# Optimization experiments

Measured on AMD Instinct MI355X. Metric: run time of the kernel, lower is better.

The kernel has to match this reference:

```python
import jax, jax.numpy as jnp
import numpy as np
from jax import lax

EPS = 1e-5  # torch LayerNorm / BatchNorm1d default eps
HEADS, DH, DEPTH, C = 4, 128, 2, 512


def setup_inputs() -> dict:
    key = jax.random.key(0)
    ks = iter(jax.random.split(key, 48))
    def rn(shape, scale=1.0):
        return jax.random.normal(next(ks), shape, jnp.float32) * scale
    d, L = 1024, DEPTH
    inp = {}
    inp['x'] = rn((16, 10, 256, d))                      # (b, ncrops, T, d)
    # Temporal embedding: Conv1d(d -> 512, k=3, pad=1) + ReLU
    inp['W_emb'] = rn((C, d, 3), (d * 3) ** -0.5)
    inp['b_emb'] = jnp.zeros((C,), jnp.float32)
    # Transformer (depth=2), params stacked along layer axis
    inp['ln1_g'] = jnp.ones((L, C), jnp.float32); inp['ln1_b'] = jnp.zeros((L, C), jnp.float32)
    inp['W_qkv'] = rn((L, C, 4 * HEADS * DH), C ** -0.5)  # to_qkv (no bias), inner_dim*4 = 2048
    inp['W_o']  = rn((L, 2 * HEADS * DH, C), (2 * HEADS * DH) ** -0.5)
    inp['b_o']  = jnp.zeros((L, C), jnp.float32)
    inp['ln2_g'] = jnp.ones((L, C), jnp.float32); inp['ln2_b'] = jnp.zeros((L, C), jnp.float32)
    inp['W_f1'] = rn((L, C, C), C ** -0.5); inp['b_f1'] = jnp.zeros((L, C), jnp.float32)
    inp['W_f2'] = rn((L, C, C), C ** -0.5); inp['b_f2'] = jnp.zeros((L, C), jnp.float32)
    # NormalHead: conv1 512->32 (k=1), bn1, conv2 32->16 (k=1), bn2, conv3 16->1 (k=1)
    inp['c1_W'] = rn((32, C), C ** -0.5); inp['c1_b'] = jnp.zeros((32,), jnp.float32)
    inp['bn1_g'] = jnp.ones((32,), jnp.float32); inp['bn1_b'] = jnp.zeros((32,), jnp.float32)
    inp['bn1_m'] = rn((32,), 0.1)
    inp['bn1_v'] = jax.random.uniform(next(ks), (32,), jnp.float32, 0.5, 1.5)
    inp['c2_W'] = rn((16, 32), 32 ** -0.5); inp['c2_b'] = jnp.zeros((16,), jnp.float32)
    inp['bn2_g'] = jnp.ones((16,), jnp.float32); inp['bn2_b'] = jnp.zeros((16,), jnp.float32)
    inp['bn2_m'] = rn((16,), 0.1)
    inp['bn2_v'] = jax.random.uniform(next(ks), (16,), jnp.float32, 0.5, 1.5)
    inp['c3_W'] = rn((1, 16), 0.25); inp['c3_b'] = jnp.zeros((1,), jnp.float32)
    return inp


def _ln(z, g, b):
    m = z.mean(-1, keepdims=True)
    v = ((z - m) ** 2).mean(-1, keepdims=True)
    return (z - m) / jnp.sqrt(v + EPS) * g + b


def _bn_eval(z, g, b, m, v):  # z: (B, C, T), eval-mode BatchNorm1d
    return (z - m[None, :, None]) / jnp.sqrt(v[None, :, None] + EPS) * g[None, :, None] + b[None, :, None]


def _k1conv(z, W, b):  # pointwise Conv1d: z (B, Ci, T), W (Co, Ci)
    return jnp.einsum('bct,oc->bot', z, W) + b[None, :, None]


def reference(x, W_emb, b_emb, ln1_g, ln1_b, W_qkv, W_o, b_o, ln2_g, ln2_b,
              W_f1, b_f1, W_f2, b_f2, c1_W, c1_b, bn1_g, bn1_b, bn1_m, bn1_v,
              c2_W, c2_b, bn2_g, bn2_b, bn2_m, bn2_v, c3_W, c3_b):
    b, n, T, d = x.shape
    h = x.reshape(b * n, T, d)
    # Temporal embedding: Conv1d(k=3, pad=1) + ReLU
    h = lax.conv_general_dilated(h.transpose(0, 2, 1), W_emb, (1,), 'SAME',
                                 dimension_numbers=('NCH', 'OIH', 'NCH'))
    h = jax.nn.relu(h + b_emb[None, :, None]).transpose(0, 2, 1)  # (BN, T, 512)

    # fixed positional-decay attention map attn2 (T, T), batch-independent
    idx = jnp.arange(T, dtype=jnp.float32)
    tg = jnp.abs(idx[None, :] - idx[:, None])
    a2 = jnp.exp(-tg / jnp.exp(1.0))
    a2 = a2 / a2.sum(-1)  # NOTE: broadcast over last axis, exactly as in the torch code

    scale = DH ** -0.5
    for l in range(DEPTH):
        z = _ln(h, ln1_g[l], ln1_b[l])
        qkvt = z @ W_qkv[l]                                   # (BN, T, 2048)
        q, k, v, t = jnp.split(qkvt, 4, axis=-1)
        def to_heads(u):
            return u.reshape(u.shape[0], T, HEADS, DH).transpose(0, 2, 1, 3)
        q, k, v, t = map(to_heads, (q, k, v, t))              # (BN, H, T, DH)
        attn1 = jax.nn.softmax(jnp.einsum('bhid,bhjd->bhij', q, k) * scale, axis=-1)
        o1 = jnp.einsum('bhij,bhjd->bhid', attn1, v)
        o2 = jnp.einsum('ij,bhjd->bhid', a2, t)
        o = jnp.concatenate([o1, o2], axis=-1)                # (BN, H, T, 2*DH)
        o = o.transpose(0, 2, 1, 3).reshape(h.shape[0], T, HEADS * 2 * DH)
        h = o @ W_o[l] + b_o[l] + h                           # attn residual
        z = _ln(h, ln2_g[l], ln2_b[l])
        h = (jax.nn.gelu(z @ W_f1[l] + b_f1[l], approximate=False) @ W_f2[l] + b_f2[l]) + h

    # NormalHead on (BN, C, T)
    f = h.transpose(0, 2, 1)
    x1 = _k1conv(f, c1_W, c1_b)                               # (BN, 32, T)
    x2 = _k1conv(jax.nn.relu(_bn_eval(x1, bn1_g, bn1_b, bn1_m, bn1_v)), c2_W, c2_b)  # (BN, 16, T)
    scores = jax.nn.sigmoid(_k1conv(jax.nn.relu(_bn_eval(x2, bn2_g, bn2_b, bn2_m, bn2_v)), c3_W, c3_b))
    normal_scores = scores.reshape(b, n, T).mean(1)           # mean over ncrops -> (b, T)

    def maha(feats, anchor, var):  # Mahalanobis distance vs BN running stats (no eps, as in source)
        dist = jnp.sqrt(jnp.sum((feats - anchor[None, :, None]) ** 2 / var[None, :, None], axis=1))
        return dist.reshape(b, n, T).mean(1)

    distance_sum = maha(x1, bn1_m, bn1_v) + maha(x2, bn2_m, bn2_v)
    return distance_sum * normal_scores                       # (b, T)
```

## Files before the change

### kernel.cpp

```cpp
#include <hip/hip_runtime.h>
#include <math.h>

#define T_    256
#define D_    1024
#define C_    512
#define H_    4
#define DH_   128
#define BNB   160
#define LEPS  1e-5f
#define INV_E 0.36787944117144233f
#define SCALE_ 0.08838834764831845f
#define LDT   40

typedef unsigned short ushort;
typedef unsigned int   uint;
typedef __attribute__((ext_vector_type(8))) short short8;
typedef __attribute__((ext_vector_type(4))) float f32x4;

__device__ __forceinline__ ushort f2b(float f) {
    uint u = __float_as_uint(f);
    u += 0x7fffu + ((u >> 16) & 1u);
    return (ushort)(u >> 16);
}
__device__ __forceinline__ float b2f(ushort u) {
    return __uint_as_float(((uint)u) << 16);
}
__device__ __forceinline__ uint pk(float a, float b) {
    return (uint)f2b(a) | ((uint)f2b(b) << 16);
}

__global__ void zero_k(float* __restrict__ p, int n) {
    int i = blockIdx.x * 256 + threadIdx.x;
    if (i < n) p[i] = 0.0f;
}

__global__ void xcvt_k(const float* __restrict__ src, ushort* __restrict__ dst, int n4) {
    int i = blockIdx.x * 256 + threadIdx.x;
    if (i < n4) {
        float4 f = ((const float4*)src)[i];
        uint2 v;
        v.x = pk(f.x, f.y);
        v.y = pk(f.z, f.w);
        ((uint2*)dst)[i] = v;
    }
}

__global__ void tconv_k(const float* __restrict__ src, ushort* __restrict__ dst,
                        int K, int N) {
    int idx = blockIdx.x * 256 + threadIdx.x;
    if (idx >= N * K) return;
    int n = idx / K, k = idx % K;
    dst[idx] = f2b(src[(size_t)k * N + n]);
}

__global__ void bcvt_k(const float* __restrict__ src, ushort* __restrict__ dst, int n) {
    int i = blockIdx.x * 256 + threadIdx.x;
    if (i < n) dst[i] = f2b(src[i]);
}

__global__ void wemb_k(const float* __restrict__ W, ushort* __restrict__ Wt) {
    int idx = blockIdx.x * 256 + threadIdx.x;
    if (idx >= C_ * 3072) return;
    int c = idx / 3072, k = idx % 3072;
    int dt = k >> 10, ci = k & 1023;
    Wt[idx] = f2b(W[(size_t)c * 3072 + ci * 3 + dt]);
}

__global__ void a2_colsum_k(float* __restrict__ s) {
    int j = threadIdx.x;
    float acc = 0.0f;
    for (int k = 0; k < T_; k++) acc += expf(-fabsf((float)(j - k)) * INV_E);
    s[j] = acc;
}

__global__ void a2fill_k(const float* __restrict__ s, ushort* __restrict__ A2) {
    int i = blockIdx.x, j = threadIdx.x;
    A2[i * 256 + j] = f2b(expf(-fabsf((float)(i - j)) * INV_E) / s[j]);
}

__global__ __launch_bounds__(256)
void ln_k(const ushort* __restrict__ X, const float* __restrict__ g,
          const float* __restrict__ b, ushort* __restrict__ Z) {
    int row = blockIdx.x;
    int tid = threadIdx.x;
    const ushort* xr = X + (size_t)row * C_;
    float x0 = b2f(xr[tid]), x1 = b2f(xr[tid + 256]);
    __shared__ float red[256];
    red[tid] = x0 + x1;
    __syncthreads();
    for (int s = 128; s >= 1; s >>= 1) {
        if (tid < s) red[tid] += red[tid + s];
        __syncthreads();
    }
    float mean = red[0] * (1.0f / C_);
    __syncthreads();
    float d0 = x0 - mean, d1 = x1 - mean;
    red[tid] = d0 * d0 + d1 * d1;
    __syncthreads();
    for (int s = 128; s >= 1; s >>= 1) {
        if (tid < s) red[tid] += red[tid + s];
        __syncthreads();
    }
    float rinv = rsqrtf(red[0] * (1.0f / C_) + LEPS);
    ushort* zr = Z + (size_t)row * C_;
    zr[tid]       = f2b(d0 * rinv * g[tid]       + b[tid]);
    zr[tid + 256] = f2b(d1 * rinv * g[tid + 256] + b[tid + 256]);
}

template<int CONV, int ACT, int RESID, int OUTBF>
__global__ __launch_bounds__(256)
void gemm_k(const ushort* __restrict__ A, const ushort* __restrict__ B,
            const float* __restrict__ bias, const ushort* __restrict__ R,
            void* __restrict__ Cout, int M, int N, int K,
            const ushort* __restrict__ Xb) {
    __shared__ __align__(16) ushort As[128 * LDT];
    __shared__ __align__(16) ushort Bs[128 * LDT];
    const int tid  = threadIdx.x;
    const int lane = tid & 63, wave = tid >> 6;
    const int wr = wave >> 1, wc = wave & 1;
    const int lm = lane & 15, quad = lane >> 4;

    const int NP = gridDim.x, My = gridDim.y;
    int m_idx, n_idx;
    if ((My & 7) == 0) {
        int bid = blockIdx.y * NP + blockIdx.x;
        m_idx = (bid & 7) + 8 * (bid / (8 * NP));
        n_idx = (bid >> 3) % NP;
    } else {
        m_idx = blockIdx.y; n_idx = blockIdx.x;
    }
    const int m0 = m_idx * 128, n0 = n_idx * 128;
    const int r  = tid >> 1;
    const int c0 = (tid & 1) * 2;

    f32x4 acc[4][4];
#pragma unroll
    for (int mt = 0; mt < 4; mt++)
#pragma unroll
        for (int nt = 0; nt < 4; nt++) acc[mt][nt] = (f32x4){0.f, 0.f, 0.f, 0.f};

    for (int k0 = 0; k0 < K; k0 += 32) {
        if (CONV) {
            int g = m0 + r, bn = g >> 8, t = g & 255;
#pragma unroll
            for (int cc = 0; cc < 2; cc++) {
                int c = c0 + cc;
                int kc = k0 + c * 8;
                int dt = kc >> 10, ci = kc & 1023;
                int tt = t + dt - 1;
                uint4 val;
                if (tt >= 0 && tt < T_) {
                    val = *(const uint4*)(Xb + ((size_t)bn * T_ + tt) * D_ + ci);
                } else {
                    val.x = 0u; val.y = 0u; val.z = 0u; val.w = 0u;
                }
                *(uint4*)&As[r * LDT + c * 8] = val;
            }
        } else {
            const ushort* Arow = A + (size_t)(m0 + r) * K + k0;
            *(uint4*)&As[r * LDT + c0 * 8]       = *(const uint4*)(Arow + c0 * 8);
            *(uint4*)&As[r * LDT + (c0 + 1) * 8] = *(const uint4*)(Arow + (c0 + 1) * 8);
        }
        {
            const ushort* Brow = B + (size_t)(n0 + r) * K + k0;
            *(uint4*)&Bs[r * LDT + c0 * 8]       = *(const uint4*)(Brow + c0 * 8);
            *(uint4*)&Bs[r * LDT + (c0 + 1) * 8] = *(const uint4*)(Brow + (c0 + 1) * 8);
        }
        __syncthreads();
        short8 af[4], bfv[4];
#pragma unroll
        for (int mt = 0; mt < 4; mt++)
            af[mt] = *(const short8*)&As[(wr * 64 + mt * 16 + lm) * LDT + quad * 8];
#pragma unroll
        for (int nt = 0; nt < 4; nt++)
            bfv[nt] = *(const short8*)&Bs[(wc * 64 + nt * 16 + lm) * LDT + quad * 8];
#pragma unroll
        for (int mt = 0; mt < 4; mt++)
#pragma unroll
            for (int nt = 0; nt < 4; nt++)
                acc[mt][nt] = __builtin_amdgcn_mfma_f32_16x16x32_bf16(
                    af[mt], bfv[nt], acc[mt][nt], 0, 0, 0);
        __syncthreads();
    }

#pragma unroll
    for (int mt = 0; mt < 4; mt++) {
        int grow0 = m0 + wr * 64 + mt * 16 + quad * 4;
#pragma unroll
        for (int nt = 0; nt < 4; nt++) {
            int gcol = n0 + wc * 64 + nt * 16 + lm;
            float bia = bias ? bias[gcol] : 0.0f;
            f32x4 v = acc[mt][nt];
#pragma unroll
            for (int i = 0; i < 4; i++) {
                int grow = grow0 + i;
                float val = v[i] + bia;
                if (ACT == 1) val = val * 0.5f * (1.0f + erff(val * 0.70710678118654752f));
                if (ACT == 2) val = fmaxf(val, 0.0f);
                if (RESID) val += b2f(R[(size_t)grow * N + gcol]);
                if (OUTBF) ((ushort*)Cout)[(size_t)grow * N + gcol] = f2b(val);
                else       ((float*)Cout)[(size_t)grow * N + gcol]  = val;
            }
        }
    }
}

__global__ __launch_bounds__(256)
void attn1_k(const ushort* __restrict__ qkvt, ushort* __restrict__ O) {
    const int bn = blockIdx.x, h = blockIdx.y;
    const int tid = threadIdx.x;
    const int wave = tid >> 6, lane = tid & 63;
    const int lm = lane & 15, quad = lane >> 4;
    __shared__ __align__(16) ushort Ks[32 * 136];
    __shared__ __align__(16) ushort Vt[128 * 40];
    __shared__ __align__(16) ushort Ps[4][64 * 40];
    const ushort* base = qkvt + (size_t)bn * T_ * 2048;

    short8 aq[4][4];
#pragma unroll
    for (int mt = 0; mt < 4; mt++) {
        const ushort* qrow = base + (size_t)(wave * 64 + mt * 16 + lm) * 2048 + h * DH_;
#pragma unroll
        for (int ks = 0; ks < 4; ks++)
            aq[mt][ks] = *(const short8*)(qrow + ks * 32 + quad * 8);
    }

    f32x4 oacc[4][8];
#pragma unroll
    for (int mt = 0; mt < 4; mt++)
#pragma unroll
        for (int nt = 0; nt < 8; nt++) oacc[mt][nt] = (f32x4){0.f, 0.f, 0.f, 0.f};
    float mrow[4][4], lrow[4][4];
#pragma unroll
    for (int mt = 0; mt < 4; mt++)
#pragma unroll
        for (int i = 0; i < 4; i++) { mrow[mt][i] = -1e30f; lrow[mt][i] = 0.0f; }

    for (int kt = 0; kt < 8; kt++) {
        __syncthreads();
#pragma unroll
        for (int u = 0; u < 2; u++) {
            int ii = tid + u * 256;
            int j = ii >> 4, dc = ii & 15;
            *(uint4*)&Ks[j * 136 + dc * 8] =
                *(const uint4*)(base + (size_t)(kt * 32 + j) * 2048 + 512 + h * DH_ + dc * 8);
        }
        {
            int j = tid & 31, half = tid >> 5;
            const ushort* vrow = base + (size_t)(kt * 32 + j) * 2048 + 1024 + h * DH_ + half * 16;
            uint4 v0 = *(const uint4*)vrow;
            uint4 v1 = *(const uint4*)(vrow + 8);
            ushort e[16];
            *(uint4*)&e[0] = v0; *(uint4*)&e[8] = v1;
#pragma unroll
            for (int u = 0; u < 16; u++)
                Vt[(half * 16 + u) * 40 + j] = e[u];
        }
        __syncthreads();

        f32x4 s[4][2];
#pragma unroll
        for (int mt = 0; mt < 4; mt++)
#pragma unroll
            for (int nt = 0; nt < 2; nt++) s[mt][nt] = (f32x4){0.f, 0.f, 0.f, 0.f};
#pragma unroll
        for (int ks = 0; ks < 4; ks++) {
            short8 bk0 = *(const short8*)&Ks[lm * 136 + ks * 32 + quad * 8];
            short8 bk1 = *(const short8*)&Ks[(16 + lm) * 136 + ks * 32 + quad * 8];
#pragma unroll
            for (int mt = 0; mt < 4; mt++) {
                s[mt][0] = __builtin_amdgcn_mfma_f32_16x16x32_bf16(aq[mt][ks], bk0, s[mt][0], 0, 0, 0);
                s[mt][1] = __builtin_amdgcn_mfma_f32_16x16x32_bf16(aq[mt][ks], bk1, s[mt][1], 0, 0, 0);
            }
        }

#pragma unroll
        for (int mt = 0; mt < 4; mt++) {
#pragma unroll
            for (int i = 0; i < 4; i++) {
                float v0 = s[mt][0][i] * SCALE_;
                float v1 = s[mt][1][i] * SCALE_;
                float rmax = fmaxf(v0, v1);
#pragma unroll
                for (int mk = 1; mk < 16; mk <<= 1)
                    rmax = fmaxf(rmax, __shfl_xor(rmax, mk));
                float mold = mrow[mt][i];
                float mnew = fmaxf(mold, rmax);
                float alpha = __expf(mold - mnew);
                float p0 = __expf(v0 - mnew);
                float p1 = __expf(v1 - mnew);
                float rs = p0 + p1;
#pragma unroll
                for (int mk = 1; mk < 16; mk <<= 1)
                    rs += __shfl_xor(rs, mk);
                lrow[mt][i] = lrow[mt][i] * alpha + rs;
                mrow[mt][i] = mnew;
#pragma unroll
                for (int nt = 0; nt < 8; nt++) {
                    oacc[mt][nt][i] *= alpha;
                }
                int prow = mt * 16 + quad * 4 + i;
                Ps[wave][prow * 40 + lm]      = f2b(p0);
                Ps[wave][prow * 40 + 16 + lm] = f2b(p1);
            }
        }

        short8 ap[4];
#pragma unroll
        for (int mt = 0; mt < 4; mt++)
            ap[mt] = *(const short8*)&Ps[wave][(mt * 16 + lm) * 40 + quad * 8];
#pragma unroll
        for (int nt = 0; nt < 8; nt++) {
            short8 bv = *(const short8*)&Vt[(nt * 16 + lm) * 40 + quad * 8];
#pragma unroll
            for (int mt = 0; mt < 4; mt++)
                oacc[mt][nt] = __builtin_amdgcn_mfma_f32_16x16x32_bf16(ap[mt], bv, oacc[mt][nt], 0, 0, 0);
        }
    }

#pragma unroll
    for (int mt = 0; mt < 4; mt++) {
#pragma unroll
        for (int i = 0; i < 4; i++) {
            int row = wave * 64 + mt * 16 + quad * 4 + i;
            float rinv = 1.0f / lrow[mt][i];
#pragma unroll
            for (int nt = 0; nt < 8; nt++) {
                int d = nt * 16 + lm;
                O[((size_t)bn * T_ + row) * 1024 + h * 256 + d] =
                    f2b(oacc[mt][nt][i] * rinv);
            }
        }
    }
}

__global__ __launch_bounds__(256)
void attn2_k(const ushort* __restrict__ A2, const ushort* __restrict__ qkvt,
             ushort* __restrict__ O) {
    __shared__ __align__(16) ushort As[128 * LDT];
    __shared__ __align__(16) ushort Bs[128 * 48];
    const int tid = threadIdx.x;
    const int bn = blockIdx.z;
    const int m0 = blockIdx.y * 128;
    const int n0 = blockIdx.x * 128;
    const int lane = tid & 63, wave = tid >> 6;
    const int wr = wave >> 1, wc = wave & 1;
    const int lm = lane & 15, quad = lane >> 4;
    const ushort* tbase = qkvt + (size_t)bn * T_ * 2048 + 1536;
    const int r = tid >> 1, c0 = (tid & 1) * 2;

    f32x4 acc[4][4];
#pragma unroll
    for (int mt = 0; mt < 4; mt++)
#pragma unroll
        for (int nt = 0; nt < 4; nt++) acc[mt][nt] = (f32x4){0.f, 0.f, 0.f, 0.f};

    for (int k0 = 0; k0 < 256; k0 += 32) {
        const ushort* Arow = A2 + (size_t)(m0 + r) * 256 + k0;
        *(uint4*)&As[r * LDT + c0 * 8]       = *(const uint4*)(Arow + c0 * 8);
        *(uint4*)&As[r * LDT + (c0 + 1) * 8] = *(const uint4*)(Arow + (c0 + 1) * 8);
        {
            int kr = tid & 31, np = tid >> 5;
            const ushort* trow = tbase + (size_t)(k0 + kr) * 2048 + n0 + np * 16;
            uint4 v0 = *(const uint4*)trow;
            uint4 v1 = *(const uint4*)(trow + 8);
            ushort e[16];
            *(uint4*)&e[0] = v0; *(uint4*)&e[8] = v1;
#pragma unroll
            for (int u = 0; u < 16; u++)
                Bs[(np * 16 + u) * 48 + kr] = e[u];
        }
        __syncthreads();
        short8 af[4], bf[4];
#pragma unroll
        for (int mt = 0; mt < 4; mt++)
            af[mt] = *(const short8*)&As[(wr * 64 + mt * 16 + lm) * LDT + quad * 8];
#pragma unroll
        for (int nt = 0; nt < 4; nt++)
            bf[nt] = *(const short8*)&Bs[(wc * 64 + nt * 16 + lm) * 48 + quad * 8];
#pragma unroll
        for (int mt = 0; mt < 4; mt++)
#pragma unroll
            for (int nt = 0; nt < 4; nt++)
                acc[mt][nt] = __builtin_amdgcn_mfma_f32_16x16x32_bf16(
                    af[mt], bf[nt], acc[mt][nt], 0, 0, 0);
        __syncthreads();
    }

#pragma unroll
    for (int mt = 0; mt < 4; mt++) {
        int row0 = m0 + wr * 64 + mt * 16 + quad * 4;
#pragma unroll
        for (int nt = 0; nt < 4; nt++) {
            int n = n0 + wc * 64 + nt * 16 + lm;
            int h = n >> 7, d = n & 127;
#pragma unroll
            for (int i = 0; i < 4; i++) {
                int row = row0 + i;
                O[((size_t)bn * T_ + row) * 1024 + h * 256 + 128 + d] =
                    f2b(acc[mt][nt][i]);
            }
        }
    }
}

#define BLD 520
__global__ __launch_bounds__(256)
void head1_k(const ushort* __restrict__ Hb, const ushort* __restrict__ c1Wb,
             const float* __restrict__ c1b, float* __restrict__ X1) {
    __shared__ __align__(16) ushort As[128 * LDT];
    __shared__ __align__(16) ushort Bs[32 * BLD];
    const int tid = threadIdx.x;
    const int lane = tid & 63, wave = tid >> 6;
    const int lm = lane & 15, quad = lane >> 4;
    const int m0 = blockIdx.x * 128;
#pragma unroll
    for (int u = 0; u < 8; u++) {
        int ii = tid + u * 256;
        int nrow = ii >> 6;
        int koff = (ii & 63) * 8;
        *(uint4*)&Bs[nrow * BLD + koff] = *(const uint4*)(c1Wb + nrow * 512 + koff);
    }
    f32x4 acc[2][2];
#pragma unroll
    for (int mt = 0; mt < 2; mt++)
#pragma unroll
        for (int nt = 0; nt < 2; nt++) acc[mt][nt] = (f32x4){0.f, 0.f, 0.f, 0.f};

    const int r = tid >> 1, half = tid & 1;
    for (int k0 = 0; k0 < 512; k0 += 32) {
        const ushort* s = Hb + (size_t)(m0 + r) * 512 + k0 + half * 16;
        uint4 v0 = *(const uint4*)s;
        uint4 v1 = *(const uint4*)(s + 8);
        __syncthreads();
        *(uint4*)&As[r * LDT + half * 16]     = v0;
        *(uint4*)&As[r * LDT + half * 16 + 8] = v1;
        __syncthreads();
        short8 af[2], bf[2];
#pragma unroll
        for (int mt = 0; mt < 2; mt++)
            af[mt] = *(const short8*)&As[(wave * 32 + mt * 16 + lm) * LDT + quad * 8];
#pragma unroll
        for (int nt = 0; nt < 2; nt++)
            bf[nt] = *(const short8*)&Bs[(nt * 16 + lm) * BLD + k0 + quad * 8];
#pragma unroll
        for (int mt = 0; mt < 2; mt++)
#pragma unroll
            for (int nt = 0; nt < 2; nt++)
                acc[mt][nt] = __builtin_amdgcn_mfma_f32_16x16x32_bf16(
                    af[mt], bf[nt], acc[mt][nt], 0, 0, 0);
    }
#pragma unroll
    for (int mt = 0; mt < 2; mt++) {
        int row0 = m0 + wave * 32 + mt * 16 + quad * 4;
#pragma unroll
        for (int nt = 0; nt < 2; nt++) {
            int col = nt * 16 + lm;
            float bia = c1b[col];
#pragma unroll
            for (int i = 0; i < 4; i++)
                X1[(size_t)(row0 + i) * 32 + col] = acc[mt][nt][i] + bia;
        }
    }
}

__global__ __launch_bounds__(256)
void head2_k(const float* __restrict__ X1, int bn_base, int M,
             const float* __restrict__ g1, const float* __restrict__ b1,
             const float* __restrict__ m1, const float* __restrict__ v1,
             const float* __restrict__ c2W, const float* __restrict__ c2b,
             const float* __restrict__ g2, const float* __restrict__ b2,
             const float* __restrict__ m2, const float* __restrict__ v2,
             const float* __restrict__ c3W, const float* __restrict__ c3b,
             float* __restrict__ sum_dist, float* __restrict__ sum_score) {
    int row = blockIdx.x * 256 + threadIdx.x;
    if (row >= M) return;
    float x1[32], y1[32];
    const float* xr = X1 + (size_t)row * 32;
#pragma unroll
    for (int c = 0; c < 32; c++) x1[c] = xr[c];
    float d1 = 0.0f;
#pragma unroll
    for (int c = 0; c < 32; c++) {
        float dd = x1[c] - m1[c];
        d1 += dd * dd / v1[c];
        y1[c] = fmaxf(0.0f, dd * rsqrtf(v1[c] + LEPS) * g1[c] + b1[c]);
    }
    float d2 = 0.0f, sc = c3b[0];
#pragma unroll
    for (int o = 0; o < 16; o++) {
        float acc = c2b[o];
        const float* wr = c2W + o * 32;
#pragma unroll
        for (int c = 0; c < 32; c++) acc += wr[c] * y1[c];
        float dd = acc - m2[o];
        d2 += dd * dd / v2[o];
        float y2 = fmaxf(0.0f, dd * rsqrtf(v2[o] + LEPS) * g2[o] + b2[o]);
        sc += c3W[o] * y2;
    }
    float dist = sqrtf(d1) + sqrtf(d2);
    sc = 1.0f / (1.0f + expf(-sc));
    int bn = bn_base + (row >> 8);
    int t = row & 255;
    int b = bn / 10;
    atomicAdd(&sum_dist[b * T_ + t], dist);
    atomicAdd(&sum_score[b * T_ + t], sc);
}

__global__ void combine_k(const float* __restrict__ sd, const float* __restrict__ ss,
                          float* __restrict__ out) {
    int i = blockIdx.x * 256 + threadIdx.x;
    if (i < 16 * T_) out[i] = (sd[i] * 0.1f) * (ss[i] * 0.1f);
}

extern "C" void kernel_launch(void* const* d_in, const int* in_sizes, int n_in,
                              void* d_out, int out_size, void* d_ws, size_t ws_size,
                              hipStream_t stream) {
    const float* x     = (const float*)d_in[0];
    const float* W_emb = (const float*)d_in[1];
    const float* b_emb = (const float*)d_in[2];
    const float* ln1_g = (const float*)d_in[3];
    const float* ln1_b = (const float*)d_in[4];
    const float* W_qkv = (const float*)d_in[5];
    const float* W_o   = (const float*)d_in[6];
    const float* b_o   = (const float*)d_in[7];
    const float* ln2_g = (const float*)d_in[8];
    const float* ln2_b = (const float*)d_in[9];
    const float* W_f1  = (const float*)d_in[10];
    const float* b_f1  = (const float*)d_in[11];
    const float* W_f2  = (const float*)d_in[12];
    const float* b_f2  = (const float*)d_in[13];
    const float* c1_W  = (const float*)d_in[14];
    const float* c1_b  = (const float*)d_in[15];
    const float* bn1_g = (const float*)d_in[16];
    const float* bn1_b = (const float*)d_in[17];
    const float* bn1_m = (const float*)d_in[18];
    const float* bn1_v = (const float*)d_in[19];
    const float* c2_W  = (const float*)d_in[20];
    const float* c2_b  = (const float*)d_in[21];
    const float* bn2_g = (const float*)d_in[22];
    const float* bn2_b = (const float*)d_in[23];
    const float* bn2_m = (const float*)d_in[24];
    const float* bn2_v = (const float*)d_in[25];
    const float* c3_W  = (const float*)d_in[26];
    const float* c3_b  = (const float*)d_in[27];
    float* out = (float*)d_out;

    char* p = (char*)d_ws;
    auto alloc = [&](size_t bytes) -> char* {
        char* q = p; p += (bytes + 255) & ~(size_t)255; return q;
    };
    ushort* wEmb = (ushort*)alloc((size_t)C_ * 3072 * 2);
    ushort* wQkv = (ushort*)alloc((size_t)2 * 2048 * 512 * 2);
    ushort* wO   = (ushort*)alloc((size_t)2 * 512 * 1024 * 2);
    ushort* wF1  = (ushort*)alloc((size_t)2 * 512 * 512 * 2);
    ushort* wF2  = (ushort*)alloc((size_t)2 * 512 * 512 * 2);
    ushort* A2bf = (ushort*)alloc((size_t)256 * 256 * 2);
    ushort* c1Wb = (ushort*)alloc((size_t)32 * 512 * 2);
    float*  s256      = (float*)alloc(256 * 4);
    float*  sum_dist  = (float*)alloc(4096 * 4);
    float*  sum_score = (float*)alloc(4096 * 4);
    size_t fixedB = (size_t)(p - (char*)d_ws);

    int CH = 8;
    const int cands[7] = {160, 80, 40, 32, 20, 16, 10};
    for (int ci = 0; ci < 7; ci++) {
        size_t per = (size_t)cands[ci] * 256 * 10368 + 8192;
        if (fixedB + per <= ws_size) { CH = cands[ci]; break; }
    }
    const int MR = CH * 256;
    ushort* xb   = (ushort*)alloc((size_t)MR * 1024 * 2);
    ushort* h    = (ushort*)alloc((size_t)MR * 512 * 2);
    ushort* z    = (ushort*)alloc((size_t)MR * 512 * 2);
    ushort* qkvt = (ushort*)alloc((size_t)MR * 2048 * 2);
    ushort* o    = (ushort*)alloc((size_t)MR * 1024 * 2);
    ushort* g    = o;
    float*  X1   = (float*)alloc((size_t)MR * 32 * 4);

    zero_k<<<(8192 + 255) / 256, 256, 0, stream>>>(sum_dist, 8192);
    a2_colsum_k<<<1, 256, 0, stream>>>(s256);
    a2fill_k<<<256, 256, 0, stream>>>(s256, A2bf);
    wemb_k<<<(C_ * 3072 + 255) / 256, 256, 0, stream>>>(W_emb, wEmb);
    bcvt_k<<<(32 * 512 + 255) / 256, 256, 0, stream>>>(c1_W, c1Wb, 32 * 512);
    for (int l = 0; l < 2; l++) {
        tconv_k<<<(2048 * 512 + 255) / 256, 256, 0, stream>>>(
            W_qkv + (size_t)l * 512 * 2048, wQkv + (size_t)l * 2048 * 512, 512, 2048);
        tconv_k<<<(512 * 1024 + 255) / 256, 256, 0, stream>>>(
            W_o + (size_t)l * 1024 * 512, wO + (size_t)l * 512 * 1024, 1024, 512);
        tconv_k<<<(512 * 512 + 255) / 256, 256, 0, stream>>>(
            W_f1 + (size_t)l * 512 * 512, wF1 + (size_t)l * 512 * 512, 512, 512);
        tconv_k<<<(512 * 512 + 255) / 256, 256, 0, stream>>>(
            W_f2 + (size_t)l * 512 * 512, wF2 + (size_t)l * 512 * 512, 512, 512);
    }

    for (int cs = 0; cs < BNB; cs += CH) {
        const float* xc = x + (size_t)cs * T_ * D_;

        int n4 = MR * 1024 / 4;
        xcvt_k<<<(n4 + 255) / 256, 256, 0, stream>>>(xc, xb, n4);

        gemm_k<1, 2, 0, 1><<<dim3(512 / 128, MR / 128), 256, 0, stream>>>(
            nullptr, wEmb, b_emb, nullptr, h, MR, 512, 3072, xb);

        for (int l = 0; l < 2; l++) {
            ln_k<<<MR, 256, 0, stream>>>(h, ln1_g + l * C_, ln1_b + l * C_, z);
            gemm_k<0, 0, 0, 1><<<dim3(2048 / 128, MR / 128), 256, 0, stream>>>(
                z, wQkv + (size_t)l * 2048 * 512, nullptr, nullptr, qkvt,
                MR, 2048, 512, nullptr);
            attn1_k<<<dim3(CH, H_), 256, 0, stream>>>(qkvt, o);
            attn2_k<<<dim3(4, 2, CH), 256, 0, stream>>>(A2bf, qkvt, o);
            gemm_k<0, 0, 1, 1><<<dim3(512 / 128, MR / 128), 256, 0, stream>>>(
                o, wO + (size_t)l * 512 * 1024, b_o + l * C_, h, h,
                MR, 512, 1024, nullptr);
            ln_k<<<MR, 256, 0, stream>>>(h, ln2_g + l * C_, ln2_b + l * C_, z);
            gemm_k<0, 1, 0, 1><<<dim3(512 / 128, MR / 128), 256, 0, stream>>>(
                z, wF1 + (size_t)l * 512 * 512, b_f1 + l * C_, nullptr, g,
                MR, 512, 512, nullptr);
            gemm_k<0, 0, 1, 1><<<dim3(512 / 128, MR / 128), 256, 0, stream>>>(
                g, wF2 + (size_t)l * 512 * 512, b_f2 + l * C_, h, h,
                MR, 512, 512, nullptr);
        }

        head1_k<<<MR / 128, 256, 0, stream>>>(h, c1Wb, c1_b, X1);
        head2_k<<<MR / 256, 256, 0, stream>>>(
            X1, cs, MR, bn1_g, bn1_b, bn1_m, bn1_v,
            c2_W, c2_b, bn2_g, bn2_b, bn2_m, bn2_v, c3_W, c3_b,
            sum_dist, sum_score);
    }

    combine_k<<<16, 256, 0, stream>>>(sum_dist, sum_score, out);
}
```

Measured before the change: 1.778 ms.

## Use direct global-to-LDS loads in GEMM, pad conv input, wave-per-row LayerNorm

The GEMM tile loads now go straight from global memory into LDS through global_load_lds, with an unpadded 32-wide LDS layout. The conv input is stored with zero halo rows, so the embedding GEMM needs no bounds checks. LayerNorm is rewritten to use one wave per row, vectorized loads and shuffle reductions in place of block-wide LDS reductions, and the weight transpose kernel now goes through a shared-memory tile. Costs: the unpadded LDS rows may cause bank conflicts on fragment reads, single-pass variance is less numerically robust, and the workspace per chunk grows slightly.

```diff
diff --git a/kernel.cpp b/kernel.cpp
--- a/kernel.cpp
+++ b/kernel.cpp
@@ -11,6 +11,7 @@
 #define INV_E 0.36787944117144233f
 #define SCALE_ 0.08838834764831845f
 #define LDT   40
+#define XROW  264192
 
 typedef unsigned short ushort;
 typedef unsigned int   uint;
@@ -27,6 +28,11 @@
 }
 __device__ __forceinline__ uint pk(float a, float b) {
     return (uint)f2b(a) | ((uint)f2b(b) << 16);
+}
+__device__ __forceinline__ void gl2lds(const void* g, void* l) {
+    __builtin_amdgcn_global_load_lds(
+        (const __attribute__((address_space(1))) void*)g,
+        (__attribute__((address_space(3))) void*)l, 16, 0, 0);
 }
 
 __global__ void zero_k(float* __restrict__ p, int n) {
@@ -41,16 +47,35 @@
         uint2 v;
         v.x = pk(f.x, f.y);
         v.y = pk(f.z, f.w);
-        ((uint2*)dst)[i] = v;
-    }
-}
-
-__global__ void tconv_k(const float* __restrict__ src, ushort* __restrict__ dst,
-                        int K, int N) {
-    int idx = blockIdx.x * 256 + threadIdx.x;
-    if (idx >= N * K) return;
-    int n = idx / K, k = idx % K;
-    dst[idx] = f2b(src[(size_t)k * N + n]);
+        int e   = i * 4;
+        int bn  = e >> 18;
+        int rem = e & 262143;
+        ((uint2*)(dst + (size_t)bn * XROW + 1024 + rem))[0] = v;
+    }
+}
+
+__global__ void xpad_k(ushort* __restrict__ dst, int nbn) {
+    int i = blockIdx.x * 256 + threadIdx.x;
+    if (i >= nbn * 1024) return;
+    int bn = i >> 10, j = i & 1023;
+    int r = j >> 9, c = j & 511;
+    uint* base = (uint*)(dst + (size_t)bn * XROW);
+    base[(r ? (XROW - 1024) / 2 : 0) + c] = 0u;
+}
+
+__global__ __launch_bounds__(256)
+void tconv_k(const float* __restrict__ src, ushort* __restrict__ dst,
+             int K, int N) {
+    __shared__ float tile[32][33];
+    int kb = blockIdx.x * 32, nb = blockIdx.y * 32;
+    int tx = threadIdx.x & 31, ty = threadIdx.x >> 5;
+#pragma unroll
+    for (int i = 0; i < 32; i += 8)
+        tile[ty + i][tx] = src[(size_t)(kb + ty + i) * N + nb + tx];
+    __syncthreads();
+#pragma unroll
+    for (int i = 0; i < 32; i += 8)
+        dst[(size_t)(nb + ty + i) * K + kb + tx] = f2b(tile[tx][ty + i]);
 }
 
 __global__ void bcvt_k(const float* __restrict__ src, ushort* __restrict__ dst, int n) {
@@ -81,30 +106,36 @@
 __global__ __launch_bounds__(256)
 void ln_k(const ushort* __restrict__ X, const float* __restrict__ g,
           const float* __restrict__ b, ushort* __restrict__ Z) {
-    int row = blockIdx.x;
-    int tid = threadIdx.x;
-    const ushort* xr = X + (size_t)row * C_;
-    float x0 = b2f(xr[tid]), x1 = b2f(xr[tid + 256]);
-    __shared__ float red[256];
-    red[tid] = x0 + x1;
-    __syncthreads();
-    for (int s = 128; s >= 1; s >>= 1) {
-        if (tid < s) red[tid] += red[tid + s];
-        __syncthreads();
-    }
-    float mean = red[0] * (1.0f / C_);
-    __syncthreads();
-    float d0 = x0 - mean, d1 = x1 - mean;
-    red[tid] = d0 * d0 + d1 * d1;
-    __syncthreads();
-    for (int s = 128; s >= 1; s >>= 1) {
-        if (tid < s) red[tid] += red[tid + s];
-        __syncthreads();
-    }
-    float rinv = rsqrtf(red[0] * (1.0f / C_) + LEPS);
-    ushort* zr = Z + (size_t)row * C_;
-    zr[tid]       = f2b(d0 * rinv * g[tid]       + b[tid]);
-    zr[tid + 256] = f2b(d1 * rinv * g[tid + 256] + b[tid + 256]);
+    int row  = blockIdx.x * 4 + (threadIdx.x >> 6);
+    int lane = threadIdx.x & 63;
+    const ushort* xr = X + (size_t)row * C_ + lane * 8;
+    uint4 raw = *(const uint4*)xr;
+    float f[8];
+    f[0] = __uint_as_float(raw.x << 16); f[1] = __uint_as_float(raw.x & 0xffff0000u);
+    f[2] = __uint_as_float(raw.y << 16); f[3] = __uint_as_float(raw.y & 0xffff0000u);
+    f[4] = __uint_as_float(raw.z << 16); f[5] = __uint_as_float(raw.z & 0xffff0000u);
+    f[6] = __uint_as_float(raw.w << 16); f[7] = __uint_as_float(raw.w & 0xffff0000u);
+    float s = 0.0f, s2 = 0.0f;
+#pragma unroll
+    for (int u = 0; u < 8; u++) { s += f[u]; s2 += f[u] * f[u]; }
+#pragma unroll
+    for (int m = 1; m < 64; m <<= 1) {
+        s  += __shfl_xor(s, m);
+        s2 += __shfl_xor(s2, m);
+    }
+    float mean = s * (1.0f / C_);
+    float var  = s2 * (1.0f / C_) - mean * mean;
+    float rinv = rsqrtf(var + LEPS);
+    const float* gp = g + lane * 8;
+    const float* bp = b + lane * 8;
+    float4 g0 = *(const float4*)gp, g1 = *(const float4*)(gp + 4);
+    float4 b0 = *(const float4*)bp, b1 = *(const float4*)(bp + 4);
+    uint4 outv;
+    outv.x = pk((f[0]-mean)*rinv*g0.x+b0.x, (f[1]-mean)*rinv*g0.y+b0.y);
+    outv.y = pk((f[2]-mean)*rinv*g0.z+b0.z, (f[3]-mean)*rinv*g0.w+b0.w);
+    outv.z = pk((f[4]-mean)*rinv*g1.x+b1.x, (f[5]-mean)*rinv*g1.y+b1.y);
+    outv.w = pk((f[6]-mean)*rinv*g1.z+b1.z, (f[7]-mean)*rinv*g1.w+b1.w);
+    *(uint4*)(Z + (size_t)row * C_ + lane * 8) = outv;
 }
 
 template<int CONV, int ACT, int RESID, int OUTBF>
@@ -112,9 +143,9 @@
 void gemm_k(const ushort* __restrict__ A, const ushort* __restrict__ B,
             const float* __restrict__ bias, const ushort* __restrict__ R,
             void* __restrict__ Cout, int M, int N, int K,
-            const ushort* __restrict__ Xb) {
-    __shared__ __align__(16) ushort As[128 * LDT];
-    __shared__ __align__(16) ushort Bs[128 * LDT];
+            const ushort* __restrict__ Xp) {
+    __shared__ __align__(16) ushort As[128 * 32];
+    __shared__ __align__(16) ushort Bs[128 * 32];
     const int tid  = threadIdx.x;
     const int lane = tid & 63, wave = tid >> 6;
     const int wr = wave >> 1, wc = wave & 1;
@@ -130,8 +161,11 @@
         m_idx = blockIdx.y; n_idx = blockIdx.x;
     }
     const int m0 = m_idx * 128, n0 = n_idx * 128;
-    const int r  = tid >> 1;
-    const int c0 = (tid & 1) * 2;
+
+    const int srow   = lane >> 2;
+    const int schunk = (lane & 3) * 8;
+    ushort* AsW = As + wave * 32 * 32;
+    ushort* BsW = Bs + wave * 32 * 32;
 
     f32x4 acc[4][4];
 #pragma unroll
@@ -141,39 +175,32 @@
 
     for (int k0 = 0; k0 < K; k0 += 32) {
         if (CONV) {
-            int g = m0 + r, bn = g >> 8, t = g & 255;
-#pragma unroll
-            for (int cc = 0; cc < 2; cc++) {
-                int c = c0 + cc;
-                int kc = k0 + c * 8;
-                int dt = kc >> 10, ci = kc & 1023;
-                int tt = t + dt - 1;
-                uint4 val;
-                if (tt >= 0 && tt < T_) {
-                    val = *(const uint4*)(Xb + ((size_t)bn * T_ + tt) * D_ + ci);
-                } else {
-                    val.x = 0u; val.y = 0u; val.z = 0u; val.w = 0u;
-                }
-                *(uint4*)&As[r * LDT + c * 8] = val;
-            }
+            int dt = k0 >> 10;
+            int ci = (k0 & 1023) + schunk;
+            int g0 = m0 + wave * 32 + srow;
+            int bn0 = g0 >> 8, t0 = g0 & 255;
+            int g1 = g0 + 16;
+            int bn1 = g1 >> 8, t1 = g1 & 255;
+            gl2lds(Xp + (size_t)bn0 * XROW + (t0 + dt) * 1024 + ci, AsW);
+            gl2lds(Xp + (size_t)bn1 * XROW + (t1 + dt) * 1024 + ci, AsW + 16 * 32);
         } else {
-            const ushort* Arow = A + (size_t)(m0 + r) * K + k0;
-            *(uint4*)&As[r * LDT + c0 * 8]       = *(const uint4*)(Arow + c0 * 8);
-            *(uint4*)&As[r * LDT + (c0 + 1) * 8] = *(const uint4*)(Arow + (c0 + 1) * 8);
+            const ushort* ga = A + (size_t)(m0 + wave * 32 + srow) * K + k0 + schunk;
+            gl2lds(ga, AsW);
+            gl2lds(ga + (size_t)16 * K, AsW + 16 * 32);
         }
         {
-            const ushort* Brow = B + (size_t)(n0 + r) * K + k0;
-            *(uint4*)&Bs[r * LDT + c0 * 8]       = *(const uint4*)(Brow + c0 * 8);
-            *(uint4*)&Bs[r * LDT + (c0 + 1) * 8] = *(const uint4*)(Brow + (c0 + 1) * 8);
+            const ushort* gb = B + (size_t)(n0 + wave * 32 + srow) * K + k0 + schunk;
+            gl2lds(gb, BsW);
+            gl2lds(gb + (size_t)16 * K, BsW + 16 * 32);
         }
         __syncthreads();
         short8 af[4], bfv[4];
 #pragma unroll
         for (int mt = 0; mt < 4; mt++)
-            af[mt] = *(const short8*)&As[(wr * 64 + mt * 16 + lm) * LDT + quad * 8];
+            af[mt] = *(const short8*)&As[(wr * 64 + mt * 16 + lm) * 32 + quad * 8];
 #pragma unroll
         for (int nt = 0; nt < 4; nt++)
-            bfv[nt] = *(const short8*)&Bs[(wc * 64 + nt * 16 + lm) * LDT + quad * 8];
+            bfv[nt] = *(const short8*)&Bs[(wc * 64 + nt * 16 + lm) * 32 + quad * 8];
 #pragma unroll
         for (int mt = 0; mt < 4; mt++)
 #pragma unroll
@@ -565,11 +592,11 @@
     int CH = 8;
     const int cands[7] = {160, 80, 40, 32, 20, 16, 10};
     for (int ci = 0; ci < 7; ci++) {
-        size_t per = (size_t)cands[ci] * 256 * 10368 + 8192;
+        size_t per = (size_t)cands[ci] * 256 * 10384 + 16384;
         if (fixedB + per <= ws_size) { CH = cands[ci]; break; }
     }
     const int MR = CH * 256;
-    ushort* xb   = (ushort*)alloc((size_t)MR * 1024 * 2);
+    ushort* xbp  = (ushort*)alloc((size_t)CH * XROW * 2);
     ushort* h    = (ushort*)alloc((size_t)MR * 512 * 2);
     ushort* z    = (ushort*)alloc((size_t)MR * 512 * 2);
     ushort* qkvt = (ushort*)alloc((size_t)MR * 2048 * 2);
@@ -583,13 +610,13 @@
     wemb_k<<<(C_ * 3072 + 255) / 256, 256, 0, stream>>>(W_emb, wEmb);
     bcvt_k<<<(32 * 512 + 255) / 256, 256, 0, stream>>>(c1_W, c1Wb, 32 * 512);
     for (int l = 0; l < 2; l++) {
-        tconv_k<<<(2048 * 512 + 255) / 256, 256, 0, stream>>>(
+        tconv_k<<<dim3(512 / 32, 2048 / 32), 256, 0, stream>>>(
             W_qkv + (size_t)l * 512 * 2048, wQkv + (size_t)l * 2048 * 512, 512, 2048);
-        tconv_k<<<(512 * 1024 + 255) / 256, 256, 0, stream>>>(
+        tconv_k<<<dim3(1024 / 32, 512 / 32), 256, 0, stream>>>(
             W_o + (size_t)l * 1024 * 512, wO + (size_t)l * 512 * 1024, 1024, 512);
-        tconv_k<<<(512 * 512 + 255) / 256, 256, 0, stream>>>(
+        tconv_k<<<dim3(512 / 32, 512 / 32), 256, 0, stream>>>(
             W_f1 + (size_t)l * 512 * 512, wF1 + (size_t)l * 512 * 512, 512, 512);
-        tconv_k<<<(512 * 512 + 255) / 256, 256, 0, stream>>>(
+        tconv_k<<<dim3(512 / 32, 512 / 32), 256, 0, stream>>>(
             W_f2 + (size_t)l * 512 * 512, wF2 + (size_t)l * 512 * 512, 512, 512);
     }
 
@@ -597,13 +624,14 @@
         const float* xc = x + (size_t)cs * T_ * D_;
 
         int n4 = MR * 1024 / 4;
-        xcvt_k<<<(n4 + 255) / 256, 256, 0, stream>>>(xc, xb, n4);
+        xcvt_k<<<(n4 + 255) / 256, 256, 0, stream>>>(xc, xbp, n4);
+        xpad_k<<<(CH * 1024 + 255) / 256, 256, 0, stream>>>(xbp, CH);
 
         gemm_k<1, 2, 0, 1><<<dim3(512 / 128, MR / 128), 256, 0, stream>>>(
-            nullptr, wEmb, b_emb, nullptr, h, MR, 512, 3072, xb);
+            nullptr, wEmb, b_emb, nullptr, h, MR, 512, 3072, xbp);
 
         for (int l = 0; l < 2; l++) {
-            ln_k<<<MR, 256, 0, stream>>>(h, ln1_g + l * C_, ln1_b + l * C_, z);
+            ln_k<<<MR / 4, 256, 0, stream>>>(h, ln1_g + l * C_, ln1_b + l * C_, z);
             gemm_k<0, 0, 0, 1><<<dim3(2048 / 128, MR / 128), 256, 0, stream>>>(
                 z, wQkv + (size_t)l * 2048 * 512, nullptr, nullptr, qkvt,
                 MR, 2048, 512, nullptr);
@@ -612,7 +640,7 @@
             gemm_k<0, 0, 1, 1><<<dim3(512 / 128, MR / 128), 256, 0, stream>>>(
                 o, wO + (size_t)l * 512 * 1024, b_o + l * C_, h, h,
                 MR, 512, 1024, nullptr);
-            ln_k<<<MR, 256, 0, stream>>>(h, ln2_g + l * C_, ln2_b + l * C_, z);
+            ln_k<<<MR / 4, 256, 0, stream>>>(h, ln2_g + l * C_, ln2_b + l * C_, z);
             gemm_k<0, 1, 0, 1><<<dim3(512 / 128, MR / 128), 256, 0, stream>>>(
                 z, wF1 + (size_t)l * 512 * 512, b_f1 + l * C_, nullptr, g,
                 MR, 512, 512, nullptr);
```

Measured after the change: 1.589 ms. -10.7%, faster.
